# Optimization experiments

Hardware: AMD Instinct MI355X
Metric: run time of the kernel (lower is better)

The kernel has to match this reference:

```python
import jax, jax.numpy as jnp
import numpy as np

VOCAB, BLOCK, D, H, E, TOPK = 50257, 2048, 1024, 8, 8, 2
HD = D // H  # head_size = 128


def _layernorm(x, g, b, eps=1e-5):
    mu = jnp.mean(x, axis=-1, keepdims=True)
    var = jnp.mean(jnp.square(x - mu), axis=-1, keepdims=True)
    return (x - mu) * jax.lax.rsqrt(var + eps) * g + b


def setup_inputs() -> dict:
    key = jax.random.key(0)
    ks = jax.random.split(key, 12)
    s = 0.02
    return {
        "idx": jax.random.randint(ks[0], (4, BLOCK), 0, VOCAB),
        "tok_table": jax.random.normal(ks[1], (VOCAB, D), jnp.float32) * s,
        "pos_table": jax.random.normal(ks[2], (BLOCK, D), jnp.float32) * s,
        "Wq": jax.random.normal(ks[3], (H, D, HD), jnp.float32) * s,
        "Wk": jax.random.normal(ks[4], (H, D, HD), jnp.float32) * s,
        "Wv": jax.random.normal(ks[5], (H, D, HD), jnp.float32) * s,
        "Wo": jax.random.normal(ks[6], (D, D), jnp.float32) * s,
        "bo": jnp.zeros((D,), jnp.float32),
        "g1": jnp.ones((D,), jnp.float32),
        "b1": jnp.zeros((D,), jnp.float32),
        "g2": jnp.ones((D,), jnp.float32),
        "b2": jnp.zeros((D,), jnp.float32),
        "Wr": jax.random.normal(ks[7], (D, E), jnp.float32) * s,
        "br": jnp.zeros((E,), jnp.float32),
        "Wn": jax.random.normal(ks[8], (D, E), jnp.float32) * s,
        "bn": jnp.zeros((E,), jnp.float32),
    }


def reference(idx, tok_table, pos_table, Wq, Wk, Wv, Wo, bo, g1, b1, g2, b2, Wr, br, Wn, bn):
    B, T = idx.shape
    x = tok_table[idx] + pos_table[:T]  # [B,T,D]

    # --- multi-head causal self-attention (dropout off / eval mode) ---
    xn = _layernorm(x, g1, b1)
    q = jnp.einsum('btc,hcd->bhtd', xn, Wq)
    k = jnp.einsum('btc,hcd->bhtd', xn, Wk)
    v = jnp.einsum('btc,hcd->bhtd', xn, Wv)
    # NOTE: original scales by C**-0.5 where C = n_embed (not head_size)
    wei = jnp.einsum('bhtd,bhsd->bhts', q, k) * (D ** -0.5)
    causal = jnp.tril(jnp.ones((T, T), bool))
    wei = jnp.where(causal, wei, -jnp.inf)
    wei = jax.nn.softmax(wei, axis=-1)
    attn = jnp.einsum('bhts,bhsd->bhtd', wei, v)  # [B,H,T,HD]
    attn = attn.transpose(0, 2, 1, 3).reshape(B, T, D)  # concat heads
    x = x + attn @ Wo + bo  # residual

    x_norm = _layernorm(x, g2, b2)

    # --- noisy top-k router ---
    logits = x_norm @ Wr + br          # [B,T,E]
    noise_logits = x_norm @ Wn + bn    # [B,T,E]
    noise = jax.random.normal(jax.random.key(42), logits.shape, logits.dtype)
    noisy = logits + noise * jax.nn.softplus(noise_logits)
    top_vals, indices = jax.lax.top_k(noisy, TOPK)  # [B,T,K]
    probs_k = jax.nn.softmax(top_vals, axis=-1)     # softmax over -inf-scattered logits == softmax over top-k
    router_probs = jnp.sum(jax.nn.one_hot(indices, E, dtype=probs_k.dtype) * probs_k[..., None], axis=-2)

    return (x_norm, router_probs, indices, x)
```

## Files before the change

### kernel.cpp

```cpp
#include <hip/hip_runtime.h>
#include <math.h>
#include <stdint.h>

typedef __attribute__((ext_vector_type(8))) _Float16 f16x8;
typedef __attribute__((ext_vector_type(4))) _Float16 f16x4;
typedef __attribute__((ext_vector_type(4))) float f32x4;

__device__ __forceinline__ void split_f16(float x, _Float16& h, _Float16& l) {
  h = (_Float16)x;
  l = (_Float16)((x - (float)h) * 2048.0f);
}

__device__ __forceinline__ void gld16(const void* g, void* l) {
  __builtin_amdgcn_global_load_lds(
      (const __attribute__((address_space(1))) void*)g,
      (__attribute__((address_space(3))) void*)l, 16, 0, 0);
}

__device__ __forceinline__ void threefry2x32_42(uint32_t x0, uint32_t x1,
                                                uint32_t& o0, uint32_t& o1) {
  const uint32_t k0 = 0u, k1 = 42u;
  const uint32_t k2 = k0 ^ k1 ^ 0x1BD11BDAu;
  x0 += k0; x1 += k1;
#define TF_R(r) { x0 += x1; x1 = (x1 << (r)) | (x1 >> (32 - (r))); x1 ^= x0; }
  TF_R(13) TF_R(15) TF_R(26) TF_R(6)
  x0 += k1; x1 += k2 + 1u;
  TF_R(17) TF_R(29) TF_R(16) TF_R(24)
  x0 += k2; x1 += k0 + 2u;
  TF_R(13) TF_R(15) TF_R(26) TF_R(6)
  x0 += k0; x1 += k1 + 3u;
  TF_R(17) TF_R(29) TF_R(16) TF_R(24)
  x0 += k1; x1 += k2 + 4u;
  TF_R(13) TF_R(15) TF_R(26) TF_R(6)
  x0 += k2; x1 += k0 + 5u;
#undef TF_R
  o0 = x0; o1 = x1;
}

__device__ __forceinline__ float jax_erfinv_f32(float x) {
  float xx = __fmul_rn(x, x);
  float w = -log1pf(-xx);
  float p;
  if (w < 5.0f) {
    w = __fadd_rn(w, -2.5f);
    p = 2.81022636e-08f;
    p = __fadd_rn(3.43273939e-07f, __fmul_rn(p, w));
    p = __fadd_rn(-3.5233877e-06f, __fmul_rn(p, w));
    p = __fadd_rn(-4.39150654e-06f, __fmul_rn(p, w));
    p = __fadd_rn(0.00021858087f, __fmul_rn(p, w));
    p = __fadd_rn(-0.00125372503f, __fmul_rn(p, w));
    p = __fadd_rn(-0.00417768164f, __fmul_rn(p, w));
    p = __fadd_rn(0.246640727f, __fmul_rn(p, w));
    p = __fadd_rn(1.50140941f, __fmul_rn(p, w));
  } else {
    w = __fadd_rn(sqrtf(w), -3.0f);
    p = -0.000200214257f;
    p = __fadd_rn(0.000100950558f, __fmul_rn(p, w));
    p = __fadd_rn(0.00134934322f, __fmul_rn(p, w));
    p = __fadd_rn(-0.00367342844f, __fmul_rn(p, w));
    p = __fadd_rn(0.00573950773f, __fmul_rn(p, w));
    p = __fadd_rn(-0.0076224613f, __fmul_rn(p, w));
    p = __fadd_rn(0.00943887047f, __fmul_rn(p, w));
    p = __fadd_rn(1.00167406f, __fmul_rn(p, w));
    p = __fadd_rn(2.83297682f, __fmul_rn(p, w));
  }
  return __fmul_rn(p, x);
}

__device__ __forceinline__ float jax_noise(uint32_t n) {
  uint32_t o0, o1;
  threefry2x32_42(0u, n, o0, o1);
  uint32_t bits = o0 ^ o1;
  uint32_t fb = (bits >> 9) | 0x3F800000u;
  float f = __fadd_rn(__uint_as_float(fb), -1.0f);
  const float lo = __uint_as_float(0xBF7FFFFFu);
  float u = __fadd_rn(__fmul_rn(f, 2.0f), lo);
  u = fmaxf(lo, u);
  return __fmul_rn(__uint_as_float(0x3FB504F3u), jax_erfinv_f32(u));
}

__device__ __forceinline__ float block_sum_256(float v, float* buf) {
  #pragma unroll
  for (int off = 32; off > 0; off >>= 1) v += __shfl_down(v, off, 64);
  int lane = threadIdx.x & 63;
  int w = threadIdx.x >> 6;
  if (lane == 0) buf[w] = v;
  __syncthreads();
  return buf[0] + buf[1] + buf[2] + buf[3];
}

__global__ __launch_bounds__(128) void k_wsplit(
    const float* __restrict__ Wq, const float* __restrict__ Wk,
    const float* __restrict__ Wv, const float* __restrict__ Wo,
    _Float16* __restrict__ wqt_h, _Float16* __restrict__ wqt_l,
    _Float16* __restrict__ wot_h, _Float16* __restrict__ wot_l) {
  int z = blockIdx.x, tid = threadIdx.x;
  const float* src;
  int ldn, n;
  _Float16 *dh, *dl;
  if (z < 24) {
    int which = z >> 3, h = z & 7;
    src = ((which == 0) ? Wq : (which == 1) ? Wk : Wv) + (size_t)h * 1024 * 128;
    ldn = 128; n = tid;
    dh = wqt_h + (size_t)z * 128 * 1024 + (size_t)n * 1024;
    dl = wqt_l + (size_t)z * 128 * 1024 + (size_t)n * 1024;
  } else {
    int zz = z - 24;
    src = Wo; ldn = 1024; n = zz * 128 + tid;
    dh = wot_h + (size_t)n * 1024;
    dl = wot_l + (size_t)n * 1024;
  }
  for (int k0 = 0; k0 < 1024; k0 += 16) {
    f16x8 hv0, hv1, lv0, lv1;
    #pragma unroll
    for (int j = 0; j < 8; ++j) {
      _Float16 hh, ll;
      split_f16(src[(size_t)(k0 + j) * ldn + n], hh, ll);
      hv0[j] = hh; lv0[j] = ll;
    }
    #pragma unroll
    for (int j = 0; j < 8; ++j) {
      _Float16 hh, ll;
      split_f16(src[(size_t)(k0 + 8 + j) * ldn + n], hh, ll);
      hv1[j] = hh; lv1[j] = ll;
    }
    *(f16x8*)(dh + k0) = hv0; *(f16x8*)(dh + k0 + 8) = hv1;
    *(f16x8*)(dl + k0) = lv0; *(f16x8*)(dl + k0 + 8) = lv1;
  }
}

__global__ __launch_bounds__(256) void k_embed_ln1(
    const int* __restrict__ idx, const float* __restrict__ tok,
    const float* __restrict__ pos, const float* __restrict__ g1,
    const float* __restrict__ b1, float* __restrict__ x_out,
    _Float16* __restrict__ xnh, _Float16* __restrict__ xnl) {
  __shared__ float bufA[4], bufB[4];
  int r = blockIdx.x;
  int t = r & 2047;
  int token = idx[r];
  int c4 = threadIdx.x;
  float4 tv = *((const float4*)(tok + (size_t)token * 1024) + c4);
  float4 pv = *((const float4*)(pos + (size_t)t * 1024) + c4);
  float4 xv = make_float4(tv.x + pv.x, tv.y + pv.y, tv.z + pv.z, tv.w + pv.w);
  *((float4*)(x_out + (size_t)r * 1024) + c4) = xv;
  float mu = block_sum_256(xv.x + xv.y + xv.z + xv.w, bufA) * (1.0f / 1024.0f);
  float d0 = xv.x - mu, d1 = xv.y - mu, d2 = xv.z - mu, d3 = xv.w - mu;
  float var = block_sum_256(d0*d0 + d1*d1 + d2*d2 + d3*d3, bufB) * (1.0f / 1024.0f);
  float rs = rsqrtf(var + 1e-5f);
  float4 gv = *((const float4*)g1 + c4);
  float4 bv = *((const float4*)b1 + c4);
  float xn0 = d0*rs*gv.x + bv.x, xn1 = d1*rs*gv.y + bv.y;
  float xn2 = d2*rs*gv.z + bv.z, xn3 = d3*rs*gv.w + bv.w;
  f16x4 hv, lv;
  _Float16 hh, ll;
  split_f16(xn0, hh, ll); hv[0] = hh; lv[0] = ll;
  split_f16(xn1, hh, ll); hv[1] = hh; lv[1] = ll;
  split_f16(xn2, hh, ll); hv[2] = hh; lv[2] = ll;
  split_f16(xn3, hh, ll); hv[3] = hh; lv[3] = ll;
  *(f16x4*)(xnh + (size_t)r * 1024 + c4 * 4) = hv;
  *(f16x4*)(xnl + (size_t)r * 1024 + c4 * 4) = lv;
}

__global__ __launch_bounds__(256) void k_ln2(
    const float* __restrict__ x, const float* __restrict__ g2,
    const float* __restrict__ b2, float* __restrict__ xn_out) {
  __shared__ float bufA[4], bufB[4];
  int r = blockIdx.x;
  int c4 = threadIdx.x;
  float4 xv = *((const float4*)(x + (size_t)r * 1024) + c4);
  float mu = block_sum_256(xv.x + xv.y + xv.z + xv.w, bufA) * (1.0f / 1024.0f);
  float d0 = xv.x - mu, d1 = xv.y - mu, d2 = xv.z - mu, d3 = xv.w - mu;
  float var = block_sum_256(d0*d0 + d1*d1 + d2*d2 + d3*d3, bufB) * (1.0f / 1024.0f);
  float rs = rsqrtf(var + 1e-5f);
  float4 gv = *((const float4*)g2 + c4);
  float4 bv = *((const float4*)b2 + c4);
  float4 xn = make_float4(d0*rs*gv.x + bv.x, d1*rs*gv.y + bv.y,
                          d2*rs*gv.z + bv.z, d3*rs*gv.w + bv.w);
  *((float4*)(xn_out + (size_t)r * 1024) + c4) = xn;
}

__global__ __launch_bounds__(256) void k_qkv(
    const _Float16* __restrict__ xnh, const _Float16* __restrict__ xnl,
    const _Float16* __restrict__ wth, const _Float16* __restrict__ wtl,
    _Float16* __restrict__ qh, _Float16* __restrict__ ql,
    _Float16* __restrict__ kh, _Float16* __restrict__ kl,
    _Float16* __restrict__ vth, _Float16* __restrict__ vtl) {
  __shared__ __align__(16) _Float16 Ah[128 * 32], Al[128 * 32];
  __shared__ __align__(16) _Float16 Bh[128 * 32], Bl[128 * 32];
  int z = blockIdx.x;
  int which = z >> 3, h = z & 7;
  int m0 = blockIdx.y * 128;
  int tid = threadIdx.x, w = tid >> 6, lane = tid & 63;
  const _Float16* bsh = wth + (size_t)z * 128 * 1024;
  const _Float16* bsl = wtl + (size_t)z * 128 * 1024;
  f32x4 om[2][8], oc[2][8];
  const f32x4 zero4 = {0.f, 0.f, 0.f, 0.f};
  #pragma unroll
  for (int mr = 0; mr < 2; ++mr)
    #pragma unroll
    for (int nb = 0; nb < 8; ++nb) { om[mr][nb] = zero4; oc[mr][nb] = zero4; }

  for (int k0 = 0; k0 < 1024; k0 += 32) {
    __syncthreads();
    #pragma unroll
    for (int i2 = 0; i2 < 2; ++i2) {
      int r = w * 32 + i2 * 16 + (lane >> 2);
      int gs = (lane & 3) ^ ((r >> 1) & 3);
      size_t ao = (size_t)(m0 + r) * 1024 + k0 + gs * 8;
      size_t bo_ = (size_t)r * 1024 + k0 + gs * 8;
      gld16(xnh + ao, &Ah[(w * 32 + i2 * 16) * 32]);
      gld16(xnl + ao, &Al[(w * 32 + i2 * 16) * 32]);
      gld16(bsh + bo_, &Bh[(w * 32 + i2 * 16) * 32]);
      gld16(bsl + bo_, &Bl[(w * 32 + i2 * 16) * 32]);
    }
    asm volatile("s_waitcnt vmcnt(0)" ::: "memory");
    __syncthreads();
    f16x8 ah[2], al[2];
    #pragma unroll
    for (int mr = 0; mr < 2; ++mr) {
      int arow = w * 32 + mr * 16 + (lane & 15);
      int ag = (lane >> 4) ^ ((arow >> 1) & 3);
      ah[mr] = *(f16x8*)&Ah[arow * 32 + ag * 8];
      al[mr] = *(f16x8*)&Al[arow * 32 + ag * 8];
    }
    #pragma unroll
    for (int nb = 0; nb < 8; ++nb) {
      int brow = nb * 16 + (lane & 15);
      int bg = (lane >> 4) ^ ((brow >> 1) & 3);
      f16x8 b8h = *(f16x8*)&Bh[brow * 32 + bg * 8];
      f16x8 b8l = *(f16x8*)&Bl[brow * 32 + bg * 8];
      #pragma unroll
      for (int mr = 0; mr < 2; ++mr) {
        om[mr][nb] = __builtin_amdgcn_mfma_f32_16x16x32_f16(ah[mr], b8h, om[mr][nb], 0, 0, 0);
        oc[mr][nb] = __builtin_amdgcn_mfma_f32_16x16x32_f16(ah[mr], b8l, oc[mr][nb], 0, 0, 0);
        oc[mr][nb] = __builtin_amdgcn_mfma_f32_16x16x32_f16(al[mr], b8h, oc[mr][nb], 0, 0, 0);
      }
    }
  }
  int bb = m0 >> 11, tb = m0 & 2047;
  if (which < 2) {
    _Float16* OH = (which == 0) ? qh : kh;
    _Float16* OL = (which == 0) ? ql : kl;
    size_t base = (size_t)(bb * 8 + h) * 2048 * 128;
    #pragma unroll
    for (int mr = 0; mr < 2; ++mr)
      #pragma unroll
      for (int r2 = 0; r2 < 4; ++r2) {
        int t = tb + w * 32 + mr * 16 + ((lane >> 4) << 2) + r2;
        size_t roff = base + (size_t)t * 128 + (lane & 15);
        #pragma unroll
        for (int nb = 0; nb < 8; ++nb) {
          float v = om[mr][nb][r2] + oc[mr][nb][r2] * (1.0f / 2048.0f);
          _Float16 hh, ll;
          split_f16(v, hh, ll);
          OH[roff + nb * 16] = hh;
          OL[roff + nb * 16] = ll;
        }
      }
  } else {
    size_t base = (size_t)(bb * 8 + h) * 128 * 2048;
    #pragma unroll
    for (int mr = 0; mr < 2; ++mr) {
      int t4 = tb + w * 32 + mr * 16 + ((lane >> 4) << 2);
      #pragma unroll
      for (int nb = 0; nb < 8; ++nb) {
        int col = nb * 16 + (lane & 15);
        size_t off = base + (size_t)col * 2048 + t4;
        f16x4 hv, lv;
        #pragma unroll
        for (int r2 = 0; r2 < 4; ++r2) {
          _Float16 hh, ll;
          split_f16(om[mr][nb][r2] + oc[mr][nb][r2] * (1.0f / 2048.0f), hh, ll);
          hv[r2] = hh; lv[r2] = ll;
        }
        *(f16x4*)(vth + off) = hv;
        *(f16x4*)(vtl + off) = lv;
      }
    }
  }
}

__global__ __launch_bounds__(256) void k_proj_res(
    const _Float16* __restrict__ ah_, const _Float16* __restrict__ al_,
    const _Float16* __restrict__ wth, const _Float16* __restrict__ wtl,
    const float* __restrict__ bo, float* __restrict__ x_io) {
  __shared__ __align__(16) _Float16 Ah[128 * 64], Al[128 * 64];
  __shared__ __align__(16) _Float16 Bh[128 * 64], Bl[128 * 64];
  int n0 = blockIdx.x * 128;
  int m0 = blockIdx.y * 128;
  int tid = threadIdx.x, w = tid >> 6, lane = tid & 63;
  f32x4 om[2][8], oc[2][8];
  const f32x4 zero4 = {0.f, 0.f, 0.f, 0.f};
  #pragma unroll
  for (int mr = 0; mr < 2; ++mr)
    #pragma unroll
    for (int nb = 0; nb < 8; ++nb) { om[mr][nb] = zero4; oc[mr][nb] = zero4; }

  for (int k0 = 0; k0 < 1024; k0 += 64) {
    __syncthreads();
    #pragma unroll
    for (int i2 = 0; i2 < 4; ++i2) {
      int r = w * 32 + i2 * 8 + (lane >> 3);
      int gs = (lane & 7) ^ (r & 7);
      size_t ao = (size_t)(m0 + r) * 1024 + k0 + gs * 8;
      size_t bo_ = (size_t)(n0 + r) * 1024 + k0 + gs * 8;
      gld16(ah_ + ao, &Ah[(w * 32 + i2 * 8) * 64]);
      gld16(al_ + ao, &Al[(w * 32 + i2 * 8) * 64]);
      gld16(wth + bo_, &Bh[(w * 32 + i2 * 8) * 64]);
      gld16(wtl + bo_, &Bl[(w * 32 + i2 * 8) * 64]);
    }
    asm volatile("s_waitcnt vmcnt(0)" ::: "memory");
    __syncthreads();
    #pragma unroll
    for (int k2 = 0; k2 < 2; ++k2) {
      f16x8 ah[2], al[2];
      #pragma unroll
      for (int mr = 0; mr < 2; ++mr) {
        int arow = w * 32 + mr * 16 + (lane & 15);
        int ag = (k2 * 4 + (lane >> 4)) ^ (arow & 7);
        ah[mr] = *(f16x8*)&Ah[arow * 64 + ag * 8];
        al[mr] = *(f16x8*)&Al[arow * 64 + ag * 8];
      }
      #pragma unroll
      for (int nb = 0; nb < 8; ++nb) {
        int brow = nb * 16 + (lane & 15);
        int bg = (k2 * 4 + (lane >> 4)) ^ (brow & 7);
        f16x8 b8h = *(f16x8*)&Bh[brow * 64 + bg * 8];
        f16x8 b8l = *(f16x8*)&Bl[brow * 64 + bg * 8];
        #pragma unroll
        for (int mr = 0; mr < 2; ++mr) {
          om[mr][nb] = __builtin_amdgcn_mfma_f32_16x16x32_f16(ah[mr], b8h, om[mr][nb], 0, 0, 0);
          oc[mr][nb] = __builtin_amdgcn_mfma_f32_16x16x32_f16(ah[mr], b8l, oc[mr][nb], 0, 0, 0);
          oc[mr][nb] = __builtin_amdgcn_mfma_f32_16x16x32_f16(al[mr], b8h, oc[mr][nb], 0, 0, 0);
        }
      }
    }
  }
  #pragma unroll
  for (int mr = 0; mr < 2; ++mr)
    #pragma unroll
    for (int nb = 0; nb < 8; ++nb) {
      int col = n0 + nb * 16 + (lane & 15);
      float bov = bo[col];
      #pragma unroll
      for (int r2 = 0; r2 < 4; ++r2) {
        int gm = m0 + w * 32 + mr * 16 + ((lane >> 4) << 2) + r2;
        float* p = x_io + (size_t)gm * 1024 + col;
        *p += om[mr][nb][r2] + oc[mr][nb][r2] * (1.0f / 2048.0f) + bov;
      }
    }
}

__global__ __launch_bounds__(256) void k_attn(
    const _Float16* __restrict__ qhp, const _Float16* __restrict__ qlp,
    const _Float16* __restrict__ khp, const _Float16* __restrict__ klp,
    const _Float16* __restrict__ vthp, const _Float16* __restrict__ vtlp,
    _Float16* __restrict__ attn_h, _Float16* __restrict__ attn_l) {
  __shared__ __align__(16) _Float16 Ksh[32 * 128];
  __shared__ __align__(16) _Float16 Ksl[32 * 128];
  __shared__ __align__(16) _Float16 Vh[128 * 32];
  __shared__ __align__(16) _Float16 Vl[128 * 32];
  __shared__ __align__(16) _Float16 Ph4[4][16 * 32];
  __shared__ __align__(16) _Float16 Pl4[4][16 * 32];

  int h = blockIdx.y, b = blockIdx.z;
  int qt = ((int)blockIdx.x + 5 * (h + 8 * b)) & 31;
  int t0 = qt << 6;
  int tid = threadIdx.x;
  int w = tid >> 6, lane = tid & 63;
  int tW = t0 + w * 16;

  size_t bh = (size_t)(b * 8 + h) * 2048 * 128;
  const _Float16* qhb = qhp + bh;
  const _Float16* qlb = qlp + bh;
  const _Float16* khb = khp + bh;
  const _Float16* klb = klp + bh;
  const _Float16* vhb = vthp + bh;
  const _Float16* vlb = vtlp + bh;
  _Float16* Ph = &Ph4[w][0];
  _Float16* Pl = &Pl4[w][0];

  size_t qoff = (size_t)(tW + (lane & 15)) * 128 + ((lane >> 4) << 3);
  f16x8 qfh[4], qfl[4];
  #pragma unroll
  for (int kk = 0; kk < 4; ++kk) {
    qfh[kk] = *(const f16x8*)(qhb + qoff + kk * 32);
    qfl[kk] = *(const f16x8*)(qlb + qoff + kk * 32);
  }

  f32x4 om[8], oc[8];
  const f32x4 zero4 = {0.f, 0.f, 0.f, 0.f};
  #pragma unroll
  for (int db = 0; db < 8; ++db) { om[db] = zero4; oc[db] = zero4; }
  float mreg[4], lreg[4];
  #pragma unroll
  for (int r2 = 0; r2 < 4; ++r2) { mreg[r2] = -INFINITY; lreg[r2] = 0.f; }

  int rowBase = tW + ((lane >> 4) << 2);

  for (int j0 = 0; j0 <= t0 + 32; j0 += 32) {
    __syncthreads();
    #pragma unroll
    for (int i2 = 0; i2 < 2; ++i2) {
      int r = w * 8 + i2 * 4 + (lane >> 4);
      int gs = (lane & 15) ^ (r & 7);
      size_t go = (size_t)(j0 + r) * 128 + gs * 8;
      gld16(khb + go, &Ksh[(w * 8 + i2 * 4) * 128]);
      gld16(klb + go, &Ksl[(w * 8 + i2 * 4) * 128]);
    }
    #pragma unroll
    for (int i2 = 0; i2 < 2; ++i2) {
      int r = w * 32 + i2 * 16 + (lane >> 2);
      int gs = (lane & 3) ^ ((r >> 1) & 3);
      size_t go = (size_t)r * 2048 + j0 + gs * 8;
      gld16(vhb + go, &Vh[(w * 32 + i2 * 16) * 32]);
      gld16(vlb + go, &Vl[(w * 32 + i2 * 16) * 32]);
    }
    asm volatile("s_waitcnt vmcnt(0)" ::: "memory");
    __syncthreads();

    f32x4 sm[2], sc[2];
    #pragma unroll
    for (int nb = 0; nb < 2; ++nb) { sm[nb] = zero4; sc[nb] = zero4; }
    #pragma unroll
    for (int kk = 0; kk < 4; ++kk) {
      #pragma unroll
      for (int nb = 0; nb < 2; ++nb) {
        int krow = nb * 16 + (lane & 15);
        int kg = (kk * 4 + (lane >> 4)) ^ (krow & 7);
        f16x8 kfh = *(f16x8*)&Ksh[krow * 128 + kg * 8];
        f16x8 kfl = *(f16x8*)&Ksl[krow * 128 + kg * 8];
        sm[nb] = __builtin_amdgcn_mfma_f32_16x16x32_f16(qfh[kk], kfh, sm[nb], 0, 0, 0);
        sc[nb] = __builtin_amdgcn_mfma_f32_16x16x32_f16(qfh[kk], kfl, sc[nb], 0, 0, 0);
        sc[nb] = __builtin_amdgcn_mfma_f32_16x16x32_f16(qfl[kk], kfh, sc[nb], 0, 0, 0);
      }
    }

    float rmax[4];
    #pragma unroll
    for (int r2 = 0; r2 < 4; ++r2) rmax[r2] = -INFINITY;
    #pragma unroll
    for (int nb = 0; nb < 2; ++nb) {
      int col = j0 + nb * 16 + (lane & 15);
      #pragma unroll
      for (int r2 = 0; r2 < 4; ++r2) {
        float sv = (sm[nb][r2] + sc[nb][r2] * (1.0f / 2048.0f)) * 0.03125f;
        sv = (col > rowBase + r2) ? -INFINITY : sv;
        sm[nb][r2] = sv;
        rmax[r2] = fmaxf(rmax[r2], sv);
      }
    }
    #pragma unroll
    for (int mk = 1; mk < 16; mk <<= 1)
      #pragma unroll
      for (int r2 = 0; r2 < 4; ++r2)
        rmax[r2] = fmaxf(rmax[r2], __shfl_xor(rmax[r2], mk, 64));
    float alpha[4], rsum[4];
    #pragma unroll
    for (int r2 = 0; r2 < 4; ++r2) {
      float mnew = fmaxf(mreg[r2], rmax[r2]);
      alpha[r2] = __expf(mreg[r2] - mnew);
      mreg[r2] = mnew;
      rsum[r2] = 0.f;
    }
    #pragma unroll
    for (int nb = 0; nb < 2; ++nb)
      #pragma unroll
      for (int r2 = 0; r2 < 4; ++r2) {
        float p = __expf(sm[nb][r2] - mreg[r2]);
        sm[nb][r2] = p;
        rsum[r2] += p;
      }
    #pragma unroll
    for (int mk = 1; mk < 16; mk <<= 1)
      #pragma unroll
      for (int r2 = 0; r2 < 4; ++r2)
        rsum[r2] += __shfl_xor(rsum[r2], mk, 64);
    #pragma unroll
    for (int r2 = 0; r2 < 4; ++r2)
      lreg[r2] = lreg[r2] * alpha[r2] + rsum[r2];

    #pragma unroll
    for (int nb = 0; nb < 2; ++nb) {
      int col = nb * 16 + (lane & 15);
      #pragma unroll
      for (int r2 = 0; r2 < 4; ++r2) {
        int prow = ((lane >> 4) << 2) + r2;
        int sg = (col >> 3) ^ ((prow >> 1) & 3);
        float ps = sm[nb][r2] * 16384.0f;
        _Float16 hh, ll;
        split_f16(ps, hh, ll);
        Ph[prow * 32 + sg * 8 + (col & 7)] = hh;
        Pl[prow * 32 + sg * 8 + (col & 7)] = ll;
      }
    }

    #pragma unroll
    for (int db = 0; db < 8; ++db)
      #pragma unroll
      for (int r2 = 0; r2 < 4; ++r2) {
        om[db][r2] *= alpha[r2];
        oc[db][r2] *= alpha[r2];
      }

    {
      int prow = lane & 15;
      int pg = (lane >> 4) ^ ((prow >> 1) & 3);
      f16x8 pah = *(f16x8*)&Ph[prow * 32 + pg * 8];
      f16x8 pal = *(f16x8*)&Pl[prow * 32 + pg * 8];
      #pragma unroll
      for (int db = 0; db < 8; ++db) {
        int vrow = db * 16 + (lane & 15);
        int vg = (lane >> 4) ^ ((vrow >> 1) & 3);
        f16x8 vfh = *(f16x8*)&Vh[vrow * 32 + vg * 8];
        f16x8 vfl = *(f16x8*)&Vl[vrow * 32 + vg * 8];
        om[db] = __builtin_amdgcn_mfma_f32_16x16x32_f16(pah, vfh, om[db], 0, 0, 0);
        oc[db] = __builtin_amdgcn_mfma_f32_16x16x32_f16(pah, vfl, oc[db], 0, 0, 0);
        oc[db] = __builtin_amdgcn_mfma_f32_16x16x32_f16(pal, vfh, oc[db], 0, 0, 0);
      }
    }
  }

  size_t obase = ((size_t)(b * 2048 + rowBase)) * 1024 + h * 128 + (lane & 15);
  #pragma unroll
  for (int r2 = 0; r2 < 4; ++r2) {
    float inv = 1.f / (lreg[r2] * 16384.0f);
    #pragma unroll
    for (int db = 0; db < 8; ++db) {
      float v = (om[db][r2] + oc[db][r2] * (1.0f / 2048.0f)) * inv;
      _Float16 hh, ll;
      split_f16(v, hh, ll);
      attn_h[obase + (size_t)r2 * 1024 + db * 16] = hh;
      attn_l[obase + (size_t)r2 * 1024 + db * 16] = ll;
    }
  }
}

__global__ __launch_bounds__(256) void k_router(
    const float* __restrict__ xn, const float* __restrict__ Wr,
    const float* __restrict__ br, const float* __restrict__ Wn,
    const float* __restrict__ bn, float* __restrict__ rp_out,
    float* __restrict__ idx_out) {
  int wave = threadIdx.x >> 6, lane = threadIdx.x & 63;
  int r = blockIdx.x * 4 + wave;
  const float* xr = xn + (size_t)r * 1024;
  float acc[16];
  #pragma unroll
  for (int i = 0; i < 16; ++i) acc[i] = 0.f;
  int cbase = lane * 16;
  for (int cc = 0; cc < 16; ++cc) {
    int c = cbase + cc;
    float xv = xr[c];
    const float4* wr4 = (const float4*)(Wr + (size_t)c * 8);
    float4 w0 = wr4[0], w1 = wr4[1];
    acc[0] += xv * w0.x; acc[1] += xv * w0.y; acc[2] += xv * w0.z; acc[3] += xv * w0.w;
    acc[4] += xv * w1.x; acc[5] += xv * w1.y; acc[6] += xv * w1.z; acc[7] += xv * w1.w;
    const float4* wn4 = (const float4*)(Wn + (size_t)c * 8);
    float4 n0 = wn4[0], n1 = wn4[1];
    acc[8]  += xv * n0.x; acc[9]  += xv * n0.y; acc[10] += xv * n0.z; acc[11] += xv * n0.w;
    acc[12] += xv * n1.x; acc[13] += xv * n1.y; acc[14] += xv * n1.z; acc[15] += xv * n1.w;
  }
  #pragma unroll
  for (int i = 0; i < 16; ++i) {
    #pragma unroll
    for (int off = 32; off > 0; off >>= 1) acc[i] += __shfl_down(acc[i], off, 64);
  }
  if (lane == 0) {
    float noisy[8];
    uint32_t nbase = (uint32_t)r * 8u;
    #pragma unroll
    for (int e = 0; e < 8; ++e) {
      float lg = acc[e] + br[e];
      float x = acc[8 + e] + bn[e];
      float sp = __fadd_rn(fmaxf(x, 0.f), log1pf(expf(-fabsf(x))));
      float nz = jax_noise(nbase + (uint32_t)e);
      noisy[e] = __fadd_rn(lg, __fmul_rn(nz, sp));
    }
    float v1 = -INFINITY, v2 = -INFINITY;
    int i1 = 0, i2 = 0;
    #pragma unroll
    for (int e = 0; e < 8; ++e) {
      float vv = noisy[e];
      if (vv > v1) { v2 = v1; i2 = i1; v1 = vv; i1 = e; }
      else if (vv > v2) { v2 = vv; i2 = e; }
    }
    float e2 = expf(v2 - v1);
    float ssum = 1.f + e2;
    float p1 = 1.f / ssum, p2 = e2 / ssum;
    float rp[8];
    #pragma unroll
    for (int e = 0; e < 8; ++e) rp[e] = 0.f;
    rp[i1] = p1; rp[i2] = p2;
    float* op = rp_out + (size_t)r * 8;
    #pragma unroll
    for (int e = 0; e < 8; ++e) op[e] = rp[e];
    idx_out[(size_t)r * 2]     = (float)i1;
    idx_out[(size_t)r * 2 + 1] = (float)i2;
  }
}

extern "C" void kernel_launch(void* const* d_in, const int* in_sizes, int n_in,
                              void* d_out, int out_size, void* d_ws, size_t ws_size,
                              hipStream_t stream) {
  const int*   idx = (const int*)d_in[0];
  const float* tok = (const float*)d_in[1];
  const float* pos = (const float*)d_in[2];
  const float* Wq  = (const float*)d_in[3];
  const float* Wk  = (const float*)d_in[4];
  const float* Wv  = (const float*)d_in[5];
  const float* Wo  = (const float*)d_in[6];
  const float* bo  = (const float*)d_in[7];
  const float* g1  = (const float*)d_in[8];
  const float* b1  = (const float*)d_in[9];
  const float* g2  = (const float*)d_in[10];
  const float* b2  = (const float*)d_in[11];
  const float* Wr  = (const float*)d_in[12];
  const float* br  = (const float*)d_in[13];
  const float* Wn  = (const float*)d_in[14];
  const float* bn  = (const float*)d_in[15];

  float* out_xnorm = (float*)d_out;
  float* out_rp    = out_xnorm + 8388608;
  float* out_idx   = out_rp + 65536;
  float* out_x     = out_idx + 16384;

  _Float16* xnh  = (_Float16*)d_ws;
  _Float16* xnl  = xnh + 8388608;
  _Float16* qhp  = xnl + 8388608;
  _Float16* qlp  = qhp + 8388608;
  _Float16* khp  = qlp + 8388608;
  _Float16* klp  = khp + 8388608;
  _Float16* vthp = klp + 8388608;
  _Float16* vtlp = vthp + 8388608;
  _Float16* attn_h = xnh;
  _Float16* attn_l = xnl;
  _Float16* wqt_h = (_Float16*)out_xnorm;
  _Float16* wqt_l = wqt_h + 3145728;
  _Float16* wot_h = wqt_l + 3145728;
  _Float16* wot_l = wot_h + 1048576;

  k_wsplit<<<32, 128, 0, stream>>>(Wq, Wk, Wv, Wo, wqt_h, wqt_l, wot_h, wot_l);
  k_embed_ln1<<<8192, 256, 0, stream>>>(idx, tok, pos, g1, b1, out_x, xnh, xnl);
  k_qkv<<<dim3(24, 64), 256, 0, stream>>>(xnh, xnl, wqt_h, wqt_l,
                                          qhp, qlp, khp, klp, vthp, vtlp);
  k_attn<<<dim3(32, 8, 4), 256, 0, stream>>>(qhp, qlp, khp, klp, vthp, vtlp,
                                             attn_h, attn_l);
  k_proj_res<<<dim3(8, 64), 256, 0, stream>>>(attn_h, attn_l, wot_h, wot_l, bo, out_x);
  k_ln2<<<8192, 256, 0, stream>>>(out_x, g2, b2, out_xnorm);
  k_router<<<2048, 256, 0, stream>>>(out_xnorm, Wr, br, Wn, bn, out_rp, out_idx);
}
```

Before: 1.081 ms.

## Double-buffer K/V tiles and pair causal query tiles per attention block

The attention kernel now double-buffers the K and V shared-memory tiles, issuing async global-to-LDS loads for the next key block while the current one is computed, so load latency is hidden behind MFMA work. Each block handles two query tiles (qs and 31-qs), which balances causal work across blocks and halves the grid. The output rescale by alpha is skipped when no row maximum changed in the wave. The cost is twice the K/V LDS footprint, which may lower occupancy, and a grid of 512 blocks that each run longer.

```diff
diff --git a/kernel.cpp b/kernel.cpp
--- a/kernel.cpp
+++ b/kernel.cpp
@@ -356,19 +356,17 @@
     const _Float16* __restrict__ khp, const _Float16* __restrict__ klp,
     const _Float16* __restrict__ vthp, const _Float16* __restrict__ vtlp,
     _Float16* __restrict__ attn_h, _Float16* __restrict__ attn_l) {
-  __shared__ __align__(16) _Float16 Ksh[32 * 128];
-  __shared__ __align__(16) _Float16 Ksl[32 * 128];
-  __shared__ __align__(16) _Float16 Vh[128 * 32];
-  __shared__ __align__(16) _Float16 Vl[128 * 32];
+  __shared__ __align__(16) _Float16 Ksh[2][32 * 128];
+  __shared__ __align__(16) _Float16 Ksl[2][32 * 128];
+  __shared__ __align__(16) _Float16 Vh[2][128 * 32];
+  __shared__ __align__(16) _Float16 Vl[2][128 * 32];
   __shared__ __align__(16) _Float16 Ph4[4][16 * 32];
   __shared__ __align__(16) _Float16 Pl4[4][16 * 32];
 
   int h = blockIdx.y, b = blockIdx.z;
-  int qt = ((int)blockIdx.x + 5 * (h + 8 * b)) & 31;
-  int t0 = qt << 6;
+  int qs = blockIdx.x;
   int tid = threadIdx.x;
   int w = tid >> 6, lane = tid & 63;
-  int tW = t0 + w * 16;
 
   size_t bh = (size_t)(b * 8 + h) * 2048 * 128;
   const _Float16* qhb = qhp + bh;
@@ -380,158 +378,182 @@
   _Float16* Ph = &Ph4[w][0];
   _Float16* Pl = &Pl4[w][0];
 
-  size_t qoff = (size_t)(tW + (lane & 15)) * 128 + ((lane >> 4) << 3);
-  f16x8 qfh[4], qfl[4];
-  #pragma unroll
-  for (int kk = 0; kk < 4; ++kk) {
-    qfh[kk] = *(const f16x8*)(qhb + qoff + kk * 32);
-    qfl[kk] = *(const f16x8*)(qlb + qoff + kk * 32);
-  }
-
-  f32x4 om[8], oc[8];
   const f32x4 zero4 = {0.f, 0.f, 0.f, 0.f};
-  #pragma unroll
-  for (int db = 0; db < 8; ++db) { om[db] = zero4; oc[db] = zero4; }
-  float mreg[4], lreg[4];
-  #pragma unroll
-  for (int r2 = 0; r2 < 4; ++r2) { mreg[r2] = -INFINITY; lreg[r2] = 0.f; }
-
-  int rowBase = tW + ((lane >> 4) << 2);
-
-  for (int j0 = 0; j0 <= t0 + 32; j0 += 32) {
-    __syncthreads();
+
+  auto stage = [&](int cur, int j0) {
     #pragma unroll
     for (int i2 = 0; i2 < 2; ++i2) {
       int r = w * 8 + i2 * 4 + (lane >> 4);
       int gs = (lane & 15) ^ (r & 7);
       size_t go = (size_t)(j0 + r) * 128 + gs * 8;
-      gld16(khb + go, &Ksh[(w * 8 + i2 * 4) * 128]);
-      gld16(klb + go, &Ksl[(w * 8 + i2 * 4) * 128]);
+      gld16(khb + go, &Ksh[cur][(w * 8 + i2 * 4) * 128]);
+      gld16(klb + go, &Ksl[cur][(w * 8 + i2 * 4) * 128]);
     }
     #pragma unroll
     for (int i2 = 0; i2 < 2; ++i2) {
       int r = w * 32 + i2 * 16 + (lane >> 2);
       int gs = (lane & 3) ^ ((r >> 1) & 3);
       size_t go = (size_t)r * 2048 + j0 + gs * 8;
-      gld16(vhb + go, &Vh[(w * 32 + i2 * 16) * 32]);
-      gld16(vlb + go, &Vl[(w * 32 + i2 * 16) * 32]);
-    }
+      gld16(vhb + go, &Vh[cur][(w * 32 + i2 * 16) * 32]);
+      gld16(vlb + go, &Vl[cur][(w * 32 + i2 * 16) * 32]);
+    }
+  };
+
+  #pragma unroll 1
+  for (int pi = 0; pi < 2; ++pi) {
+    int qt = pi ? (31 - qs) : qs;
+    int t0 = qt << 6;
+    int tW = t0 + w * 16;
+    int rowBase = tW + ((lane >> 4) << 2);
+
+    size_t qoff = (size_t)(tW + (lane & 15)) * 128 + ((lane >> 4) << 3);
+    f16x8 qfh[4], qfl[4];
+    #pragma unroll
+    for (int kk = 0; kk < 4; ++kk) {
+      qfh[kk] = *(const f16x8*)(qhb + qoff + kk * 32);
+      qfl[kk] = *(const f16x8*)(qlb + qoff + kk * 32);
+    }
+
+    f32x4 om[8], oc[8];
+    #pragma unroll
+    for (int db = 0; db < 8; ++db) { om[db] = zero4; oc[db] = zero4; }
+    float mreg[4], lreg[4];
+    #pragma unroll
+    for (int r2 = 0; r2 < 4; ++r2) { mreg[r2] = -INFINITY; lreg[r2] = 0.f; }
+
+    int nt = 2 * qt + 2;
+    stage(0, 0);
     asm volatile("s_waitcnt vmcnt(0)" ::: "memory");
     __syncthreads();
-
-    f32x4 sm[2], sc[2];
-    #pragma unroll
-    for (int nb = 0; nb < 2; ++nb) { sm[nb] = zero4; sc[nb] = zero4; }
-    #pragma unroll
-    for (int kk = 0; kk < 4; ++kk) {
+    int cur = 0;
+
+    #pragma unroll 1
+    for (int t = 0; t < nt; ++t) {
+      if (t + 1 < nt) stage(cur ^ 1, (t + 1) * 32);
+      int j0 = t * 32;
+
+      f32x4 sm[2], sc[2];
+      #pragma unroll
+      for (int nb = 0; nb < 2; ++nb) { sm[nb] = zero4; sc[nb] = zero4; }
+      #pragma unroll
+      for (int kk = 0; kk < 4; ++kk) {
+        #pragma unroll
+        for (int nb = 0; nb < 2; ++nb) {
+          int krow = nb * 16 + (lane & 15);
+          int kg = (kk * 4 + (lane >> 4)) ^ (krow & 7);
+          f16x8 kfh = *(f16x8*)&Ksh[cur][krow * 128 + kg * 8];
+          f16x8 kfl = *(f16x8*)&Ksl[cur][krow * 128 + kg * 8];
+          sm[nb] = __builtin_amdgcn_mfma_f32_16x16x32_f16(qfh[kk], kfh, sm[nb], 0, 0, 0);
+          sc[nb] = __builtin_amdgcn_mfma_f32_16x16x32_f16(qfh[kk], kfl, sc[nb], 0, 0, 0);
+          sc[nb] = __builtin_amdgcn_mfma_f32_16x16x32_f16(qfl[kk], kfh, sc[nb], 0, 0, 0);
+        }
+      }
+
+      float rmax[4];
+      #pragma unroll
+      for (int r2 = 0; r2 < 4; ++r2) rmax[r2] = -INFINITY;
       #pragma unroll
       for (int nb = 0; nb < 2; ++nb) {
-        int krow = nb * 16 + (lane & 15);
-        int kg = (kk * 4 + (lane >> 4)) ^ (krow & 7);
-        f16x8 kfh = *(f16x8*)&Ksh[krow * 128 + kg * 8];
-        f16x8 kfl = *(f16x8*)&Ksl[krow * 128 + kg * 8];
-        sm[nb] = __builtin_amdgcn_mfma_f32_16x16x32_f16(qfh[kk], kfh, sm[nb], 0, 0, 0);
-        sc[nb] = __builtin_amdgcn_mfma_f32_16x16x32_f16(qfh[kk], kfl, sc[nb], 0, 0, 0);
-        sc[nb] = __builtin_amdgcn_mfma_f32_16x16x32_f16(qfl[kk], kfh, sc[nb], 0, 0, 0);
-      }
-    }
-
-    float rmax[4];
-    #pragma unroll
-    for (int r2 = 0; r2 < 4; ++r2) rmax[r2] = -INFINITY;
-    #pragma unroll
-    for (int nb = 0; nb < 2; ++nb) {
-      int col = j0 + nb * 16 + (lane & 15);
+        int col = j0 + nb * 16 + (lane & 15);
+        #pragma unroll
+        for (int r2 = 0; r2 < 4; ++r2) {
+          float sv = (sm[nb][r2] + sc[nb][r2] * (1.0f / 2048.0f)) * 0.03125f;
+          sv = (col > rowBase + r2) ? -INFINITY : sv;
+          sm[nb][r2] = sv;
+          rmax[r2] = fmaxf(rmax[r2], sv);
+        }
+      }
+      #pragma unroll
+      for (int mk = 1; mk < 16; mk <<= 1)
+        #pragma unroll
+        for (int r2 = 0; r2 < 4; ++r2)
+          rmax[r2] = fmaxf(rmax[r2], __shfl_xor(rmax[r2], mk, 64));
+      float alpha[4], rsum[4];
+      bool newmax = false;
       #pragma unroll
       for (int r2 = 0; r2 < 4; ++r2) {
-        float sv = (sm[nb][r2] + sc[nb][r2] * (1.0f / 2048.0f)) * 0.03125f;
-        sv = (col > rowBase + r2) ? -INFINITY : sv;
-        sm[nb][r2] = sv;
-        rmax[r2] = fmaxf(rmax[r2], sv);
-      }
-    }
-    #pragma unroll
-    for (int mk = 1; mk < 16; mk <<= 1)
+        float mnew = fmaxf(mreg[r2], rmax[r2]);
+        newmax |= (mnew > mreg[r2]);
+        alpha[r2] = __expf(mreg[r2] - mnew);
+        mreg[r2] = mnew;
+        rsum[r2] = 0.f;
+      }
+      #pragma unroll
+      for (int nb = 0; nb < 2; ++nb)
+        #pragma unroll
+        for (int r2 = 0; r2 < 4; ++r2) {
+          float p = __expf(sm[nb][r2] - mreg[r2]);
+          sm[nb][r2] = p;
+          rsum[r2] += p;
+        }
+      #pragma unroll
+      for (int mk = 1; mk < 16; mk <<= 1)
+        #pragma unroll
+        for (int r2 = 0; r2 < 4; ++r2)
+          rsum[r2] += __shfl_xor(rsum[r2], mk, 64);
       #pragma unroll
       for (int r2 = 0; r2 < 4; ++r2)
-        rmax[r2] = fmaxf(rmax[r2], __shfl_xor(rmax[r2], mk, 64));
-    float alpha[4], rsum[4];
+        lreg[r2] = lreg[r2] * alpha[r2] + rsum[r2];
+
+      #pragma unroll
+      for (int nb = 0; nb < 2; ++nb) {
+        int col = nb * 16 + (lane & 15);
+        #pragma unroll
+        for (int r2 = 0; r2 < 4; ++r2) {
+          int prow = ((lane >> 4) << 2) + r2;
+          int sg = (col >> 3) ^ ((prow >> 1) & 3);
+          float ps = sm[nb][r2] * 16384.0f;
+          _Float16 hh, ll;
+          split_f16(ps, hh, ll);
+          Ph[prow * 32 + sg * 8 + (col & 7)] = hh;
+          Pl[prow * 32 + sg * 8 + (col & 7)] = ll;
+        }
+      }
+
+      if (__any((int)newmax)) {
+        #pragma unroll
+        for (int db = 0; db < 8; ++db)
+          #pragma unroll
+          for (int r2 = 0; r2 < 4; ++r2) {
+            om[db][r2] *= alpha[r2];
+            oc[db][r2] *= alpha[r2];
+          }
+      }
+
+      {
+        int prow = lane & 15;
+        int pg = (lane >> 4) ^ ((prow >> 1) & 3);
+        f16x8 pah = *(f16x8*)&Ph[prow * 32 + pg * 8];
+        f16x8 pal = *(f16x8*)&Pl[prow * 32 + pg * 8];
+        #pragma unroll
+        for (int db = 0; db < 8; ++db) {
+          int vrow = db * 16 + (lane & 15);
+          int vg = (lane >> 4) ^ ((vrow >> 1) & 3);
+          f16x8 vfh = *(f16x8*)&Vh[cur][vrow * 32 + vg * 8];
+          f16x8 vfl = *(f16x8*)&Vl[cur][vrow * 32 + vg * 8];
+          om[db] = __builtin_amdgcn_mfma_f32_16x16x32_f16(pah, vfh, om[db], 0, 0, 0);
+          oc[db] = __builtin_amdgcn_mfma_f32_16x16x32_f16(pah, vfl, oc[db], 0, 0, 0);
+          oc[db] = __builtin_amdgcn_mfma_f32_16x16x32_f16(pal, vfh, oc[db], 0, 0, 0);
+        }
+      }
+
+      asm volatile("s_waitcnt vmcnt(0)" ::: "memory");
+      __syncthreads();
+      cur ^= 1;
+    }
+
+    size_t obase = ((size_t)(b * 2048 + rowBase)) * 1024 + h * 128 + (lane & 15);
     #pragma unroll
     for (int r2 = 0; r2 < 4; ++r2) {
-      float mnew = fmaxf(mreg[r2], rmax[r2]);
-      alpha[r2] = __expf(mreg[r2] - mnew);
-      mreg[r2] = mnew;
-      rsum[r2] = 0.f;
-    }
-    #pragma unroll
-    for (int nb = 0; nb < 2; ++nb)
-      #pragma unroll
-      for (int r2 = 0; r2 < 4; ++r2) {
-        float p = __expf(sm[nb][r2] - mreg[r2]);
-        sm[nb][r2] = p;
-        rsum[r2] += p;
-      }
-    #pragma unroll
-    for (int mk = 1; mk < 16; mk <<= 1)
-      #pragma unroll
-      for (int r2 = 0; r2 < 4; ++r2)
-        rsum[r2] += __shfl_xor(rsum[r2], mk, 64);
-    #pragma unroll
-    for (int r2 = 0; r2 < 4; ++r2)
-      lreg[r2] = lreg[r2] * alpha[r2] + rsum[r2];
-
-    #pragma unroll
-    for (int nb = 0; nb < 2; ++nb) {
-      int col = nb * 16 + (lane & 15);
-      #pragma unroll
-      for (int r2 = 0; r2 < 4; ++r2) {
-        int prow = ((lane >> 4) << 2) + r2;
-        int sg = (col >> 3) ^ ((prow >> 1) & 3);
-        float ps = sm[nb][r2] * 16384.0f;
+      float inv = 1.f / (lreg[r2] * 16384.0f);
+      #pragma unroll
+      for (int db = 0; db < 8; ++db) {
+        float v = (om[db][r2] + oc[db][r2] * (1.0f / 2048.0f)) * inv;
         _Float16 hh, ll;
-        split_f16(ps, hh, ll);
-        Ph[prow * 32 + sg * 8 + (col & 7)] = hh;
-        Pl[prow * 32 + sg * 8 + (col & 7)] = ll;
-      }
-    }
-
-    #pragma unroll
-    for (int db = 0; db < 8; ++db)
-      #pragma unroll
-      for (int r2 = 0; r2 < 4; ++r2) {
-        om[db][r2] *= alpha[r2];
-        oc[db][r2] *= alpha[r2];
-      }
-
-    {
-      int prow = lane & 15;
-      int pg = (lane >> 4) ^ ((prow >> 1) & 3);
-      f16x8 pah = *(f16x8*)&Ph[prow * 32 + pg * 8];
-      f16x8 pal = *(f16x8*)&Pl[prow * 32 + pg * 8];
-      #pragma unroll
-      for (int db = 0; db < 8; ++db) {
-        int vrow = db * 16 + (lane & 15);
-        int vg = (lane >> 4) ^ ((vrow >> 1) & 3);
-        f16x8 vfh = *(f16x8*)&Vh[vrow * 32 + vg * 8];
-        f16x8 vfl = *(f16x8*)&Vl[vrow * 32 + vg * 8];
-        om[db] = __builtin_amdgcn_mfma_f32_16x16x32_f16(pah, vfh, om[db], 0, 0, 0);
-        oc[db] = __builtin_amdgcn_mfma_f32_16x16x32_f16(pah, vfl, oc[db], 0, 0, 0);
-        oc[db] = __builtin_amdgcn_mfma_f32_16x16x32_f16(pal, vfh, oc[db], 0, 0, 0);
-      }
-    }
-  }
-
-  size_t obase = ((size_t)(b * 2048 + rowBase)) * 1024 + h * 128 + (lane & 15);
-  #pragma unroll
-  for (int r2 = 0; r2 < 4; ++r2) {
-    float inv = 1.f / (lreg[r2] * 16384.0f);
-    #pragma unroll
-    for (int db = 0; db < 8; ++db) {
-      float v = (om[db][r2] + oc[db][r2] * (1.0f / 2048.0f)) * inv;
-      _Float16 hh, ll;
-      split_f16(v, hh, ll);
-      attn_h[obase + (size_t)r2 * 1024 + db * 16] = hh;
-      attn_l[obase + (size_t)r2 * 1024 + db * 16] = ll;
+        split_f16(v, hh, ll);
+        attn_h[obase + (size_t)r2 * 1024 + db * 16] = hh;
+        attn_l[obase + (size_t)r2 * 1024 + db * 16] = ll;
+      }
     }
   }
 }
@@ -643,7 +665,7 @@
   k_embed_ln1<<<8192, 256, 0, stream>>>(idx, tok, pos, g1, b1, out_x, xnh, xnl);
   k_qkv<<<dim3(24, 64), 256, 0, stream>>>(xnh, xnl, wqt_h, wqt_l,
                                           qhp, qlp, khp, klp, vthp, vtlp);
-  k_attn<<<dim3(32, 8, 4), 256, 0, stream>>>(qhp, qlp, khp, klp, vthp, vtlp,
+  k_attn<<<dim3(16, 8, 4), 256, 0, stream>>>(qhp, qlp, khp, klp, vthp, vtlp,
                                              attn_h, attn_l);
   k_proj_res<<<dim3(8, 64), 256, 0, stream>>>(attn_h, attn_l, wot_h, wot_l, bo, out_x);
   k_ln2<<<8192, 256, 0, stream>>>(out_x, g2, b2, out_xnorm);
```

Result: no change. 1.085 ms (+0.4%).
